# Kernel tuning notes

Measured on AMD Instinct MI355X. Metric: run time of the kernel, lower is better.

The kernel has to match this reference:

```python
import jax, jax.numpy as jnp
import numpy as np

NEG_INF = -1e9  # Keras uses a large negative for masked logits


def setup_inputs() -> dict:
    key = jax.random.key(0)
    k1, k2, k3, k4, k5 = jax.random.split(key, 5)
    B, Tq, Tv, D, U = 8, 128, 128, 512, 1024
    query = jax.random.normal(k1, (B, Tq, D), dtype=jnp.float32)
    value = jax.random.normal(k2, (B, Tv, D), dtype=jnp.float32)
    mask = jnp.ones((B, Tv), dtype=bool)
    # Dense(units, use_bias=False) kernels and AdditiveAttention scale vector
    W1 = jax.random.normal(k3, (D, U), dtype=jnp.float32) * (1.0 / np.sqrt(D))
    W2 = jax.random.normal(k4, (D, U), dtype=jnp.float32) * (1.0 / np.sqrt(D))
    scale = jax.random.normal(k5, (U,), dtype=jnp.float32) * (1.0 / np.sqrt(U))
    return {"query": query, "value": value, "mask": mask,
            "W1": W1, "W2": W2, "scale": scale}


def reference(query, value, mask, W1, W2, scale):
    # Projections (Dense, no bias)
    wq = jnp.einsum('btd,du->btu', query, W1)   # [B, Tq, U]
    wk = jnp.einsum('bsd,du->bsu', value, W2)   # [B, Tv, U]
    # Additive (Bahdanau) scores: sum_u scale_u * tanh(wq + wk)
    # Materializes [B, Tq, Tv, U] broadcast-add like Keras AdditiveAttention.
    scores = jnp.einsum('u,btsu->bts', scale,
                        jnp.tanh(wq[:, :, None, :] + wk[:, None, :, :]))
    # value mask over key axis (query_mask is all-ones in the source -> no-op)
    scores = jnp.where(mask[:, None, :], scores, NEG_INF)
    attn = jax.nn.softmax(scores, axis=-1)       # [B, Tq, Tv]
    context = jnp.einsum('bts,bsd->btd', attn, value)  # [B, Tq, D]
    return context, attn
```

## Files before the change

### kernel.cpp

```cpp
#include <hip/hip_runtime.h>

#define B_  8
#define TQ  128
#define TV  128
#define DIM 512
#define UU  1024
#define NSPLIT 16
#define NP  (B_ * TQ * TV)
#define C2  2.885390081777927f

typedef __attribute__((ext_vector_type(8))) short     short8;
typedef __attribute__((ext_vector_type(4))) float     f32x4;
typedef __attribute__((ext_vector_type(4))) unsigned short us4;

__device__ __forceinline__ unsigned short bf16_rtne(float x) {
    unsigned u = __float_as_uint(x);
    unsigned r = u + 0x7FFF + ((u >> 16) & 1);
    return (unsigned short)(r >> 16);
}

__global__ __launch_bounds__(256) void k_prep(
    const float* __restrict__ Q, const float* __restrict__ Vv,
    const float* __restrict__ W1, const float* __restrict__ W2,
    unsigned short* __restrict__ Ab, unsigned short* __restrict__ Wh)
{
    __shared__ float ts[32][36];
    const int bx = blockIdx.x;
    const int t  = threadIdx.x;

    if (bx < 1024) {
        int idx = bx * 256 + t;
        int mat = idx >> 17;
        const float* src = mat ? Vv : Q;
        int off = (idx & 131071) * 4;
        float4 v = *(const float4*)&src[off];
        us4 h;
        h.x = bf16_rtne(v.x);
        h.y = bf16_rtne(v.y);
        h.z = bf16_rtne(v.z);
        h.w = bf16_rtne(v.w);
        *(us4*)&Ab[mat * 524288 + off] = h;
    } else {
        int b2   = bx - 1024;
        int mat  = b2 >> 9;
        int tile = b2 & 511;
        int n0 = (tile & 31) * 32;
        int k0 = (tile >> 5) * 32;
        const float* W = mat ? W2 : W1;

        int kk = t >> 3, n4 = (t & 7) * 4;
        float4 w = *(const float4*)&W[(k0 + kk) * UU + n0 + n4];
        ts[n4 + 0][kk] = w.x; ts[n4 + 1][kk] = w.y;
        ts[n4 + 2][kk] = w.z; ts[n4 + 3][kk] = w.w;
        __syncthreads();

        int nn = t >> 3, k4 = (t & 7) * 4;
        float4 v = *(const float4*)&ts[nn][k4];
        us4 h;
        h.x = bf16_rtne(v.x);
        h.y = bf16_rtne(v.y);
        h.z = bf16_rtne(v.z);
        h.w = bf16_rtne(v.w);
        unsigned off = mat * 524288 + (n0 + nn) * 512 + k0 + k4;
        *(us4*)&Wh[off] = h;
    }
}

#define PKP 72
__global__ __launch_bounds__(256) void k_proj(
    const unsigned short* __restrict__ Ab, const unsigned short* __restrict__ Bh,
    float* __restrict__ Eq, float* __restrict__ Ek)
{
    __shared__ short sAb[64 * PKP], sBh[64 * PKP];

    const int tid  = threadIdx.x;
    const int wave = tid >> 6;
    const int lane = tid & 63;

    const int flat = blockIdx.x;
    const int x    = flat & 7;
    const int j    = flat >> 3;
    const int pair = x * 4 + (j >> 4);
    const int nt   = pair & 15;
    const int mat  = pair >> 4;
    const int mt   = j & 15;
    const int m0   = mt * 64;
    const int n0   = nt * 64;

    const unsigned mb = mat * 524288u;
    const int wm = (wave & 1) * 32;
    const int wn = (wave >> 1) * 32;

    const int sm = tid >> 2, sg = tid & 3;
    const unsigned short* gA = Ab + mb + (m0 + sm) * 512;
    const unsigned short* gB = Bh + mb + (n0 + sm) * 512;
    const int so0 = sm * PKP + sg * 8;
    const int so1 = sm * PKP + 32 + sg * 8;

    const int fr = lane & 15, fq = lane >> 4;
    const int aOff0 = (wm + fr) * PKP + fq * 8;
    const int aOff1 = (wm + 16 + fr) * PKP + fq * 8;
    const int bOff0 = (wn + fr) * PKP + fq * 8;
    const int bOff1 = (wn + 16 + fr) * PKP + fq * 8;

    f32x4 acc00 = {0.f, 0.f, 0.f, 0.f};
    f32x4 acc01 = {0.f, 0.f, 0.f, 0.f};
    f32x4 acc10 = {0.f, 0.f, 0.f, 0.f};
    f32x4 acc11 = {0.f, 0.f, 0.f, 0.f};

    int4 rA0, rA1, rB0, rB1;
    #define LOADALL(K)                                                       \
        rA0 = *(const int4*)(gA + (K) + sg * 8);                             \
        rA1 = *(const int4*)(gA + (K) + 32 + sg * 8);                        \
        rB0 = *(const int4*)(gB + (K) + sg * 8);                             \
        rB1 = *(const int4*)(gB + (K) + 32 + sg * 8);

    LOADALL(0)

    #pragma unroll 1
    for (int kc = 0; kc < 8; ++kc) {
        *(int4*)&sAb[so0] = rA0;  *(int4*)&sAb[so1] = rA1;
        *(int4*)&sBh[so0] = rB0;  *(int4*)&sBh[so1] = rB1;
        __syncthreads();

        if (kc < 7) { LOADALL((kc + 1) * 64) }

        #pragma unroll
        for (int ks = 0; ks < 2; ++ks) {
            const int o = ks * 32;
            short8 a0 = *(const short8*)&sAb[aOff0 + o];
            short8 a1 = *(const short8*)&sAb[aOff1 + o];
            short8 b0 = *(const short8*)&sBh[bOff0 + o];
            short8 b1 = *(const short8*)&sBh[bOff1 + o];

            acc00 = __builtin_amdgcn_mfma_f32_16x16x32_bf16(a0, b0, acc00, 0, 0, 0);
            acc01 = __builtin_amdgcn_mfma_f32_16x16x32_bf16(a0, b1, acc01, 0, 0, 0);
            acc10 = __builtin_amdgcn_mfma_f32_16x16x32_bf16(a1, b0, acc10, 0, 0, 0);
            acc11 = __builtin_amdgcn_mfma_f32_16x16x32_bf16(a1, b1, acc11, 0, 0, 0);
        }
        __syncthreads();
    }
    #undef LOADALL

    float* C = mat ? Ek : Eq;
    #pragma unroll
    for (int r = 0; r < 4; ++r) {
        int row0 = m0 + wm + fq * 4 + r;
        int row1 = row0 + 16;
        int col0 = n0 + wn + fr;
        C[row0 * UU + col0]      = __builtin_amdgcn_exp2f(C2 * acc00[r]);
        C[row0 * UU + col0 + 16] = __builtin_amdgcn_exp2f(C2 * acc01[r]);
        C[row1 * UU + col0]      = __builtin_amdgcn_exp2f(C2 * acc10[r]);
        C[row1 * UU + col0 + 16] = __builtin_amdgcn_exp2f(C2 * acc11[r]);
    }
}
#undef PKP

__global__ __launch_bounds__(256) void k_scores(
    const float* __restrict__ Eq, const float* __restrict__ Ek,
    const float* __restrict__ scale, float* __restrict__ part)
{
    __shared__ float qs[64][68];
    __shared__ float ks[64][68];
    __shared__ float ss[64];

    const int tid = threadIdx.x;
    const int tx  = tid & 15;
    const int ty  = tid >> 4;
    const int b   = blockIdx.z & 7;
    const int us  = blockIdx.z >> 3;
    const int t0  = blockIdx.y * 64;
    const int s0  = blockIdx.x * 64;
    const int u0  = us * (UU / NSPLIT);

    {
        const int r  = tid >> 2;
        const int c0 = (tid & 3) * 16;
        const float* srq = &Eq[(b * TQ + t0 + r) * UU + u0 + c0];
        const float* srk = &Ek[(b * TV + s0 + r) * UU + u0 + c0];
        const int rp = (r >> 2) | ((r & 3) << 4);
        #pragma unroll
        for (int i = 0; i < 4; ++i) {
            *(float4*)&qs[r][c0 + i * 4]  = *(const float4*)(srq + i * 4);
            *(float4*)&ks[rp][c0 + i * 4] = *(const float4*)(srk + i * 4);
        }
        if (tid < 16)
            *(float4*)&ss[tid * 4] = *(const float4*)&scale[u0 + tid * 4];
    }
    __syncthreads();

    float acc[4][4] = {};

    #pragma unroll 2
    for (int u4 = 0; u4 < 16; ++u4) {
        float4 q[4], k[4];
        #pragma unroll
        for (int i = 0; i < 4; ++i)
            q[i] = *(const float4*)&qs[ty * 4 + i][u4 * 4];
        #pragma unroll
        for (int jj = 0; jj < 4; ++jj)
            k[jj] = *(const float4*)&ks[tx + (jj << 4)][u4 * 4];
        float4 sv = *(const float4*)&ss[u4 * 4];

        #pragma unroll
        for (int i = 0; i < 4; ++i) {
            #pragma unroll
            for (int jj = 0; jj < 4; ++jj) {
                float p1 = q[i].x * k[jj].x, p2 = q[i].y * k[jj].y;
                float b1 = p1 + 1.f,        b2 = p2 + 1.f;
                float n1 = fmaf(sv.y, b1, sv.x * b2);
                acc[i][jj] = fmaf(n1, __builtin_amdgcn_rcpf(b1 * b2), acc[i][jj]);
                float p3 = q[i].z * k[jj].z, p4 = q[i].w * k[jj].w;
                float b3 = p3 + 1.f,        b4 = p4 + 1.f;
                float n2 = fmaf(sv.w, b3, sv.z * b4);
                acc[i][jj] = fmaf(n2, __builtin_amdgcn_rcpf(b3 * b4), acc[i][jj]);
            }
        }
    }

    #pragma unroll
    for (int i = 0; i < 4; ++i) {
        float4 o = {acc[i][0], acc[i][1], acc[i][2], acc[i][3]};
        *(float4*)&part[us * NP + (b * TQ + t0 + ty * 4 + i) * TV + s0 + tx * 4] = o;
    }
}

__global__ __launch_bounds__(256) void k_ctx(
    const float* __restrict__ part, const int* __restrict__ mask,
    const float* __restrict__ Vv,
    float* __restrict__ attn, float* __restrict__ ctx)
{
    __shared__ float at[128][12];

    const int tid = threadIdx.x;
    const int dc  = blockIdx.x;
    const int tt  = blockIdx.y;
    const int b   = blockIdx.z;
    const int t0  = tt * 8;
    const int rg  = tid >> 5;
    const int ln  = tid & 31;
    const int base = (b * TQ + t0 + rg) * TV;

    float x[4];
    #pragma unroll
    for (int j = 0; j < 4; ++j) {
        const int s = ln + 32 * j;
        float p = 0.f;
        #pragma unroll
        for (int i = 0; i < NSPLIT; ++i) p += part[i * NP + base + s];
        x[j] = mask[b * TV + s] ? -2.f * p : -1e9f;
    }
    float m = fmaxf(fmaxf(x[0], x[1]), fmaxf(x[2], x[3]));
    #pragma unroll
    for (int o = 16; o > 0; o >>= 1) m = fmaxf(m, __shfl_xor(m, o, 64));
    const float L2E = 1.4426950408889634f;
    float e[4], sum = 0.f;
    #pragma unroll
    for (int j = 0; j < 4; ++j) {
        e[j] = __builtin_amdgcn_exp2f((x[j] - m) * L2E);
        sum += e[j];
    }
    #pragma unroll
    for (int o = 16; o > 0; o >>= 1) sum += __shfl_xor(sum, o, 64);
    const float r = __builtin_amdgcn_rcpf(sum);
    #pragma unroll
    for (int j = 0; j < 4; ++j) {
        const float a = e[j] * r;
        at[ln + 32 * j][rg] = a;
        if (dc == 0) attn[base + ln + 32 * j] = a;
    }
    __syncthreads();

    const int d  = (tid & 127) + dc * 128;
    const int tg = tid >> 7;
    float acc[4] = {};
    const float* vp = &Vv[b * TV * DIM + d];
    #pragma unroll 4
    for (int s = 0; s < TV; ++s) {
        float v  = vp[s * DIM];
        float4 a = *(const float4*)&at[s][tg * 4];
        acc[0] = fmaf(a.x, v, acc[0]);
        acc[1] = fmaf(a.y, v, acc[1]);
        acc[2] = fmaf(a.z, v, acc[2]);
        acc[3] = fmaf(a.w, v, acc[3]);
    }
    #pragma unroll
    for (int j = 0; j < 4; ++j) {
        int t = t0 + tg * 4 + j;
        ctx[(b * TQ + t) * DIM + d] = acc[j];
    }
}

extern "C" void kernel_launch(void* const* d_in, const int* in_sizes, int n_in,
                              void* d_out, int out_size, void* d_ws, size_t ws_size,
                              hipStream_t stream)
{
    const float* query = (const float*)d_in[0];
    const float* value = (const float*)d_in[1];
    const int*   mask  = (const int*)d_in[2];
    const float* W1    = (const float*)d_in[3];
    const float* W2    = (const float*)d_in[4];
    const float* scale = (const float*)d_in[5];

    float* out  = (float*)d_out;
    float* ctx  = out;
    float* attn = out + B_ * TQ * DIM;

    float* Eq   = (float*)d_ws;
    float* Ek   = Eq + 1024 * 1024;
    float* part = Ek + 1024 * 1024;
    unsigned short* Ab = (unsigned short*)(part + NSPLIT * NP);
    unsigned short* Wh = Ab + 2 * 1024 * 512;

    hipLaunchKernelGGL(k_prep,   dim3(2048),             dim3(256), 0, stream,
                       query, value, W1, W2, Ab, Wh);
    hipLaunchKernelGGL(k_proj,   dim3(512),              dim3(256), 0, stream,
                       Ab, Wh, Eq, Ek);
    hipLaunchKernelGGL(k_scores, dim3(2, 2, 8 * NSPLIT), dim3(256), 0, stream,
                       Eq, Ek, scale, part);
    hipLaunchKernelGGL(k_ctx,    dim3(4, 16, 8),         dim3(256), 0, stream,
                       part, mask, value, attn, ctx);
}
```

Measured before the change: 109.9 us.

## Double threads per block in scores and context kernels, vectorize partial reduction

The scores kernel now runs 512 threads per block, each computing a 2x4 output tile instead of 4x4, with fused multiply-add for the tanh-rational terms. The context kernel handles 16 query rows per 512-thread block and reads partial sums and mask as float4/int4 vectors. The aim is more wavefronts to hide latency and fewer memory transactions, at the cost of less register-level reuse per thread in the scores kernel.

```diff
diff --git a/kernel.cpp b/kernel.cpp
--- a/kernel.cpp
+++ b/kernel.cpp
@@ -156,7 +156,7 @@
 }
 #undef PKP
 
-__global__ __launch_bounds__(256) void k_scores(
+__global__ __launch_bounds__(512, 4) void k_scores(
     const float* __restrict__ Eq, const float* __restrict__ Ek,
     const float* __restrict__ scale, float* __restrict__ part)
 {
@@ -174,44 +174,42 @@
     const int u0  = us * (UU / NSPLIT);
 
     {
-        const int r  = tid >> 2;
-        const int c0 = (tid & 3) * 16;
+        const int r  = tid >> 3;
+        const int c0 = (tid & 7) * 8;
         const float* srq = &Eq[(b * TQ + t0 + r) * UU + u0 + c0];
         const float* srk = &Ek[(b * TV + s0 + r) * UU + u0 + c0];
         const int rp = (r >> 2) | ((r & 3) << 4);
-        #pragma unroll
-        for (int i = 0; i < 4; ++i) {
-            *(float4*)&qs[r][c0 + i * 4]  = *(const float4*)(srq + i * 4);
-            *(float4*)&ks[rp][c0 + i * 4] = *(const float4*)(srk + i * 4);
-        }
+        *(float4*)&qs[r][c0]      = *(const float4*)(srq);
+        *(float4*)&qs[r][c0 + 4]  = *(const float4*)(srq + 4);
+        *(float4*)&ks[rp][c0]     = *(const float4*)(srk);
+        *(float4*)&ks[rp][c0 + 4] = *(const float4*)(srk + 4);
         if (tid < 16)
             *(float4*)&ss[tid * 4] = *(const float4*)&scale[u0 + tid * 4];
     }
     __syncthreads();
 
-    float acc[4][4] = {};
+    float acc[2][4] = {};
 
     #pragma unroll 2
     for (int u4 = 0; u4 < 16; ++u4) {
-        float4 q[4], k[4];
-        #pragma unroll
-        for (int i = 0; i < 4; ++i)
-            q[i] = *(const float4*)&qs[ty * 4 + i][u4 * 4];
+        float4 q[2], k[4];
+        q[0] = *(const float4*)&qs[ty * 2][u4 * 4];
+        q[1] = *(const float4*)&qs[ty * 2 + 1][u4 * 4];
         #pragma unroll
         for (int jj = 0; jj < 4; ++jj)
             k[jj] = *(const float4*)&ks[tx + (jj << 4)][u4 * 4];
         float4 sv = *(const float4*)&ss[u4 * 4];
 
         #pragma unroll
-        for (int i = 0; i < 4; ++i) {
+        for (int i = 0; i < 2; ++i) {
             #pragma unroll
             for (int jj = 0; jj < 4; ++jj) {
-                float p1 = q[i].x * k[jj].x, p2 = q[i].y * k[jj].y;
-                float b1 = p1 + 1.f,        b2 = p2 + 1.f;
+                float b1 = fmaf(q[i].x, k[jj].x, 1.f);
+                float b2 = fmaf(q[i].y, k[jj].y, 1.f);
                 float n1 = fmaf(sv.y, b1, sv.x * b2);
                 acc[i][jj] = fmaf(n1, __builtin_amdgcn_rcpf(b1 * b2), acc[i][jj]);
-                float p3 = q[i].z * k[jj].z, p4 = q[i].w * k[jj].w;
-                float b3 = p3 + 1.f,        b4 = p4 + 1.f;
+                float b3 = fmaf(q[i].z, k[jj].z, 1.f);
+                float b4 = fmaf(q[i].w, k[jj].w, 1.f);
                 float n2 = fmaf(sv.w, b3, sv.z * b4);
                 acc[i][jj] = fmaf(n2, __builtin_amdgcn_rcpf(b3 * b4), acc[i][jj]);
             }
@@ -219,40 +217,45 @@
     }
 
     #pragma unroll
-    for (int i = 0; i < 4; ++i) {
+    for (int i = 0; i < 2; ++i) {
         float4 o = {acc[i][0], acc[i][1], acc[i][2], acc[i][3]};
-        *(float4*)&part[us * NP + (b * TQ + t0 + ty * 4 + i) * TV + s0 + tx * 4] = o;
-    }
-}
-
-__global__ __launch_bounds__(256) void k_ctx(
+        *(float4*)&part[us * NP + (b * TQ + t0 + ty * 2 + i) * TV + s0 + tx * 4] = o;
+    }
+}
+
+__global__ __launch_bounds__(512) void k_ctx(
     const float* __restrict__ part, const int* __restrict__ mask,
     const float* __restrict__ Vv,
     float* __restrict__ attn, float* __restrict__ ctx)
 {
-    __shared__ float at[128][12];
+    __shared__ float at[128][20];
 
     const int tid = threadIdx.x;
     const int dc  = blockIdx.x;
     const int tt  = blockIdx.y;
     const int b   = blockIdx.z;
-    const int t0  = tt * 8;
-    const int rg  = tid >> 5;
-    const int ln  = tid & 31;
+    const int t0  = tt * 16;
+
+    const int rg = tid >> 5;
+    const int ln = tid & 31;
     const int base = (b * TQ + t0 + rg) * TV;
 
+    float4 p4 = {0.f, 0.f, 0.f, 0.f};
+    #pragma unroll
+    for (int i = 0; i < NSPLIT; ++i) {
+        float4 v = *(const float4*)&part[i * NP + base + ln * 4];
+        p4.x += v.x; p4.y += v.y; p4.z += v.z; p4.w += v.w;
+    }
+    const int4 mk = *(const int4*)&mask[b * TV + ln * 4];
     float x[4];
-    #pragma unroll
-    for (int j = 0; j < 4; ++j) {
-        const int s = ln + 32 * j;
-        float p = 0.f;
-        #pragma unroll
-        for (int i = 0; i < NSPLIT; ++i) p += part[i * NP + base + s];
-        x[j] = mask[b * TV + s] ? -2.f * p : -1e9f;
-    }
+    x[0] = mk.x ? -2.f * p4.x : -1e9f;
+    x[1] = mk.y ? -2.f * p4.y : -1e9f;
+    x[2] = mk.z ? -2.f * p4.z : -1e9f;
+    x[3] = mk.w ? -2.f * p4.w : -1e9f;
+
     float m = fmaxf(fmaxf(x[0], x[1]), fmaxf(x[2], x[3]));
     #pragma unroll
-    for (int o = 16; o > 0; o >>= 1) m = fmaxf(m, __shfl_xor(m, o, 64));
+    for (int o = 16; o > 0; o >>= 1) m = fmaxf(m, __shfl_xor(m, o, 32));
     const float L2E = 1.4426950408889634f;
     float e[4], sum = 0.f;
     #pragma unroll
@@ -261,14 +264,15 @@
         sum += e[j];
     }
     #pragma unroll
-    for (int o = 16; o > 0; o >>= 1) sum += __shfl_xor(sum, o, 64);
+    for (int o = 16; o > 0; o >>= 1) sum += __shfl_xor(sum, o, 32);
     const float r = __builtin_amdgcn_rcpf(sum);
-    #pragma unroll
-    for (int j = 0; j < 4; ++j) {
-        const float a = e[j] * r;
-        at[ln + 32 * j][rg] = a;
-        if (dc == 0) attn[base + ln + 32 * j] = a;
-    }
+
+    float4 av = {e[0] * r, e[1] * r, e[2] * r, e[3] * r};
+    at[ln * 4 + 0][rg] = av.x;
+    at[ln * 4 + 1][rg] = av.y;
+    at[ln * 4 + 2][rg] = av.z;
+    at[ln * 4 + 3][rg] = av.w;
+    if (dc == 0) *(float4*)&attn[base + ln * 4] = av;
     __syncthreads();
 
     const int d  = (tid & 127) + dc * 128;
@@ -316,8 +320,8 @@
                        query, value, W1, W2, Ab, Wh);
     hipLaunchKernelGGL(k_proj,   dim3(512),              dim3(256), 0, stream,
                        Ab, Wh, Eq, Ek);
-    hipLaunchKernelGGL(k_scores, dim3(2, 2, 8 * NSPLIT), dim3(256), 0, stream,
+    hipLaunchKernelGGL(k_scores, dim3(2, 2, 8 * NSPLIT), dim3(512), 0, stream,
                        Eq, Ek, scale, part);
-    hipLaunchKernelGGL(k_ctx,    dim3(4, 16, 8),         dim3(256), 0, stream,
+    hipLaunchKernelGGL(k_ctx,    dim3(4, 8, 8),          dim3(512), 0, stream,
                        part, mask, value, attn, ctx);
 }
```

Measured after the change: 110.3 us. Within noise of the previous version (+0.3%).

## Fuse bf16 conversion into projection and merge scores, softmax, context kernels

Applied to the files above, without the earlier changes.

Removes the separate prep kernel by converting fp32 inputs and weights to bf16 inside the projection GEMM's shared-memory staging, with the weight transpose done through scalar LDS stores. Also fuses the score, softmax and context stages into one kernel per (batch, 4-query block), using packed f32x2 FMA for the score math. This drops the split-U partial buffer and two launches. The trade-off is fewer blocks (256) and each block redoing the full U=1024 reduction serially, with every block reloading Ek for its batch.

```diff
diff --git a/kernel.cpp b/kernel.cpp
--- a/kernel.cpp
+++ b/kernel.cpp
@@ -5,12 +5,11 @@
 #define TV  128
 #define DIM 512
 #define UU  1024
-#define NSPLIT 16
-#define NP  (B_ * TQ * TV)
 #define C2  2.885390081777927f
 
 typedef __attribute__((ext_vector_type(8))) short     short8;
 typedef __attribute__((ext_vector_type(4))) float     f32x4;
+typedef __attribute__((ext_vector_type(2))) float     f32x2;
 typedef __attribute__((ext_vector_type(4))) unsigned short us4;
 
 __device__ __forceinline__ unsigned short bf16_rtne(float x) {
@@ -19,56 +18,23 @@
     return (unsigned short)(r >> 16);
 }
 
-__global__ __launch_bounds__(256) void k_prep(
+__device__ __forceinline__ us4 cvt4(float4 v) {
+    us4 h;
+    h.x = bf16_rtne(v.x);
+    h.y = bf16_rtne(v.y);
+    h.z = bf16_rtne(v.z);
+    h.w = bf16_rtne(v.w);
+    return h;
+}
+
+__device__ __forceinline__ f32x2 pkfma(f32x2 a, f32x2 b, f32x2 c) {
+    return __builtin_elementwise_fma(a, b, c);
+}
+
+#define PKP 72
+__global__ __launch_bounds__(256, 2) void k_proj(
     const float* __restrict__ Q, const float* __restrict__ Vv,
     const float* __restrict__ W1, const float* __restrict__ W2,
-    unsigned short* __restrict__ Ab, unsigned short* __restrict__ Wh)
-{
-    __shared__ float ts[32][36];
-    const int bx = blockIdx.x;
-    const int t  = threadIdx.x;
-
-    if (bx < 1024) {
-        int idx = bx * 256 + t;
-        int mat = idx >> 17;
-        const float* src = mat ? Vv : Q;
-        int off = (idx & 131071) * 4;
-        float4 v = *(const float4*)&src[off];
-        us4 h;
-        h.x = bf16_rtne(v.x);
-        h.y = bf16_rtne(v.y);
-        h.z = bf16_rtne(v.z);
-        h.w = bf16_rtne(v.w);
-        *(us4*)&Ab[mat * 524288 + off] = h;
-    } else {
-        int b2   = bx - 1024;
-        int mat  = b2 >> 9;
-        int tile = b2 & 511;
-        int n0 = (tile & 31) * 32;
-        int k0 = (tile >> 5) * 32;
-        const float* W = mat ? W2 : W1;
-
-        int kk = t >> 3, n4 = (t & 7) * 4;
-        float4 w = *(const float4*)&W[(k0 + kk) * UU + n0 + n4];
-        ts[n4 + 0][kk] = w.x; ts[n4 + 1][kk] = w.y;
-        ts[n4 + 2][kk] = w.z; ts[n4 + 3][kk] = w.w;
-        __syncthreads();
-
-        int nn = t >> 3, k4 = (t & 7) * 4;
-        float4 v = *(const float4*)&ts[nn][k4];
-        us4 h;
-        h.x = bf16_rtne(v.x);
-        h.y = bf16_rtne(v.y);
-        h.z = bf16_rtne(v.z);
-        h.w = bf16_rtne(v.w);
-        unsigned off = mat * 524288 + (n0 + nn) * 512 + k0 + k4;
-        *(us4*)&Wh[off] = h;
-    }
-}
-
-#define PKP 72
-__global__ __launch_bounds__(256) void k_proj(
-    const unsigned short* __restrict__ Ab, const unsigned short* __restrict__ Bh,
     float* __restrict__ Eq, float* __restrict__ Ek)
 {
     __shared__ short sAb[64 * PKP], sBh[64 * PKP];
@@ -87,15 +53,19 @@
     const int m0   = mt * 64;
     const int n0   = nt * 64;
 
-    const unsigned mb = mat * 524288u;
+    const float* Asrc = mat ? Vv : Q;
+    const float* Wsrc = mat ? W2 : W1;
+
     const int wm = (wave & 1) * 32;
     const int wn = (wave >> 1) * 32;
 
     const int sm = tid >> 2, sg = tid & 3;
-    const unsigned short* gA = Ab + mb + (m0 + sm) * 512;
-    const unsigned short* gB = Bh + mb + (n0 + sm) * 512;
+    const float* gA = Asrc + (m0 + sm) * 512;
     const int so0 = sm * PKP + sg * 8;
     const int so1 = sm * PKP + 32 + sg * 8;
+
+    const int kk = tid & 63, ng = tid >> 6;
+    const float* gW = Wsrc + n0 + ng * 16;
 
     const int fr = lane & 15, fq = lane >> 4;
     const int aOff0 = (wm + fr) * PKP + fq * 8;
@@ -108,19 +78,38 @@
     f32x4 acc10 = {0.f, 0.f, 0.f, 0.f};
     f32x4 acc11 = {0.f, 0.f, 0.f, 0.f};
 
-    int4 rA0, rA1, rB0, rB1;
+    float4 a0, a1, a2, a3, w0, w1, w2, w3;
     #define LOADALL(K)                                                       \
-        rA0 = *(const int4*)(gA + (K) + sg * 8);                             \
-        rA1 = *(const int4*)(gA + (K) + 32 + sg * 8);                        \
-        rB0 = *(const int4*)(gB + (K) + sg * 8);                             \
-        rB1 = *(const int4*)(gB + (K) + 32 + sg * 8);
+        a0 = *(const float4*)(gA + (K) + sg * 8);                            \
+        a1 = *(const float4*)(gA + (K) + sg * 8 + 4);                        \
+        a2 = *(const float4*)(gA + (K) + 32 + sg * 8);                       \
+        a3 = *(const float4*)(gA + (K) + 32 + sg * 8 + 4);                   \
+        {                                                                    \
+            const float* wr = gW + ((K) + kk) * UU;                          \
+            w0 = *(const float4*)(wr);                                       \
+            w1 = *(const float4*)(wr + 4);                                   \
+            w2 = *(const float4*)(wr + 8);                                   \
+            w3 = *(const float4*)(wr + 12);                                  \
+        }
 
     LOADALL(0)
 
     #pragma unroll 1
     for (int kc = 0; kc < 8; ++kc) {
-        *(int4*)&sAb[so0] = rA0;  *(int4*)&sAb[so1] = rA1;
-        *(int4*)&sBh[so0] = rB0;  *(int4*)&sBh[so1] = rB1;
+        *(us4*)&sAb[so0]     = cvt4(a0);
+        *(us4*)&sAb[so0 + 4] = cvt4(a1);
+        *(us4*)&sAb[so1]     = cvt4(a2);
+        *(us4*)&sAb[so1 + 4] = cvt4(a3);
+        {
+            us4 h[4] = {cvt4(w0), cvt4(w1), cvt4(w2), cvt4(w3)};
+            #pragma unroll
+            for (int g = 0; g < 4; ++g) {
+                sBh[(ng * 16 + g * 4 + 0) * PKP + kk] = (short)h[g].x;
+                sBh[(ng * 16 + g * 4 + 1) * PKP + kk] = (short)h[g].y;
+                sBh[(ng * 16 + g * 4 + 2) * PKP + kk] = (short)h[g].z;
+                sBh[(ng * 16 + g * 4 + 3) * PKP + kk] = (short)h[g].w;
+            }
+        }
         __syncthreads();
 
         if (kc < 7) { LOADALL((kc + 1) * 64) }
@@ -128,15 +117,15 @@
         #pragma unroll
         for (int ks = 0; ks < 2; ++ks) {
             const int o = ks * 32;
-            short8 a0 = *(const short8*)&sAb[aOff0 + o];
-            short8 a1 = *(const short8*)&sAb[aOff1 + o];
-            short8 b0 = *(const short8*)&sBh[bOff0 + o];
-            short8 b1 = *(const short8*)&sBh[bOff1 + o];
-
-            acc00 = __builtin_amdgcn_mfma_f32_16x16x32_bf16(a0, b0, acc00, 0, 0, 0);
-            acc01 = __builtin_amdgcn_mfma_f32_16x16x32_bf16(a0, b1, acc01, 0, 0, 0);
-            acc10 = __builtin_amdgcn_mfma_f32_16x16x32_bf16(a1, b0, acc10, 0, 0, 0);
-            acc11 = __builtin_amdgcn_mfma_f32_16x16x32_bf16(a1, b1, acc11, 0, 0, 0);
+            short8 fa0 = *(const short8*)&sAb[aOff0 + o];
+            short8 fa1 = *(const short8*)&sAb[aOff1 + o];
+            short8 fb0 = *(const short8*)&sBh[bOff0 + o];
+            short8 fb1 = *(const short8*)&sBh[bOff1 + o];
+
+            acc00 = __builtin_amdgcn_mfma_f32_16x16x32_bf16(fa0, fb0, acc00, 0, 0, 0);
+            acc01 = __builtin_amdgcn_mfma_f32_16x16x32_bf16(fa0, fb1, acc01, 0, 0, 0);
+            acc10 = __builtin_amdgcn_mfma_f32_16x16x32_bf16(fa1, fb0, acc10, 0, 0, 0);
+            acc11 = __builtin_amdgcn_mfma_f32_16x16x32_bf16(fa1, fb1, acc11, 0, 0, 0);
         }
         __syncthreads();
     }
@@ -156,140 +145,124 @@
 }
 #undef PKP
 
-__global__ __launch_bounds__(256) void k_scores(
+#define EKP 132
+__global__ __launch_bounds__(256, 2) void k_sac(
     const float* __restrict__ Eq, const float* __restrict__ Ek,
-    const float* __restrict__ scale, float* __restrict__ part)
-{
-    __shared__ float qs[64][68];
-    __shared__ float ks[64][68];
-    __shared__ float ss[64];
-
-    const int tid = threadIdx.x;
-    const int tx  = tid & 15;
-    const int ty  = tid >> 4;
-    const int b   = blockIdx.z & 7;
-    const int us  = blockIdx.z >> 3;
-    const int t0  = blockIdx.y * 64;
-    const int s0  = blockIdx.x * 64;
-    const int u0  = us * (UU / NSPLIT);
-
-    {
-        const int r  = tid >> 2;
-        const int c0 = (tid & 3) * 16;
-        const float* srq = &Eq[(b * TQ + t0 + r) * UU + u0 + c0];
-        const float* srk = &Ek[(b * TV + s0 + r) * UU + u0 + c0];
-        const int rp = (r >> 2) | ((r & 3) << 4);
-        #pragma unroll
-        for (int i = 0; i < 4; ++i) {
-            *(float4*)&qs[r][c0 + i * 4]  = *(const float4*)(srq + i * 4);
-            *(float4*)&ks[rp][c0 + i * 4] = *(const float4*)(srk + i * 4);
-        }
-        if (tid < 16)
-            *(float4*)&ss[tid * 4] = *(const float4*)&scale[u0 + tid * 4];
-    }
-    __syncthreads();
-
-    float acc[4][4] = {};
-
-    #pragma unroll 2
-    for (int u4 = 0; u4 < 16; ++u4) {
-        float4 q[4], k[4];
-        #pragma unroll
-        for (int i = 0; i < 4; ++i)
-            q[i] = *(const float4*)&qs[ty * 4 + i][u4 * 4];
-        #pragma unroll
-        for (int jj = 0; jj < 4; ++jj)
-            k[jj] = *(const float4*)&ks[tx + (jj << 4)][u4 * 4];
-        float4 sv = *(const float4*)&ss[u4 * 4];
-
-        #pragma unroll
-        for (int i = 0; i < 4; ++i) {
-            #pragma unroll
-            for (int jj = 0; jj < 4; ++jj) {
-                float p1 = q[i].x * k[jj].x, p2 = q[i].y * k[jj].y;
-                float b1 = p1 + 1.f,        b2 = p2 + 1.f;
-                float n1 = fmaf(sv.y, b1, sv.x * b2);
-                acc[i][jj] = fmaf(n1, __builtin_amdgcn_rcpf(b1 * b2), acc[i][jj]);
-                float p3 = q[i].z * k[jj].z, p4 = q[i].w * k[jj].w;
-                float b3 = p3 + 1.f,        b4 = p4 + 1.f;
-                float n2 = fmaf(sv.w, b3, sv.z * b4);
-                acc[i][jj] = fmaf(n2, __builtin_amdgcn_rcpf(b3 * b4), acc[i][jj]);
-            }
-        }
-    }
-
-    #pragma unroll
-    for (int i = 0; i < 4; ++i) {
-        float4 o = {acc[i][0], acc[i][1], acc[i][2], acc[i][3]};
-        *(float4*)&part[us * NP + (b * TQ + t0 + ty * 4 + i) * TV + s0 + tx * 4] = o;
-    }
-}
-
-__global__ __launch_bounds__(256) void k_ctx(
-    const float* __restrict__ part, const int* __restrict__ mask,
+    const float* __restrict__ scale, const int* __restrict__ mask,
     const float* __restrict__ Vv,
     float* __restrict__ attn, float* __restrict__ ctx)
 {
-    __shared__ float at[128][12];
+    __shared__ float ek2[64][EKP];
+    __shared__ float qs[4][68];
+    __shared__ float ss[64];
+    __shared__ float at[4][132];
 
     const int tid = threadIdx.x;
-    const int dc  = blockIdx.x;
-    const int tt  = blockIdx.y;
-    const int b   = blockIdx.z;
-    const int t0  = tt * 8;
-    const int rg  = tid >> 5;
-    const int ln  = tid & 31;
-    const int base = (b * TQ + t0 + rg) * TV;
-
-    float x[4];
+    const int bid = blockIdx.x;
+    const int b   = bid & 7;
+    const int t0  = (bid >> 3) * 4;
+    const int sp  = tid & 63;
+    const int tq  = tid >> 6;
+
+    const int uu = tid >> 6;
+    const float* ekrow0 = &Ek[(b * TV + 2 * sp) * UU + uu * 16];
+    const float* ekrow1 = ekrow0 + UU;
+
+    f32x2 acc = {0.f, 0.f};
+    const f32x2 one2 = {1.f, 1.f};
+
+    #pragma unroll 1
+    for (int uc = 0; uc < 16; ++uc) {
+        const int u0 = uc * 64;
+        if (uc) __syncthreads();
+        #pragma unroll
+        for (int c = 0; c < 4; ++c) {
+            float4 ra = *(const float4*)(ekrow0 + u0 + c * 4);
+            float4 rb = *(const float4*)(ekrow1 + u0 + c * 4);
+            float4 lo = {ra.x, rb.x, ra.y, rb.y};
+            float4 hi = {ra.z, rb.z, ra.w, rb.w};
+            *(float4*)&ek2[sp][(uu * 16 + c * 4) * 2]     = lo;
+            *(float4*)&ek2[sp][(uu * 16 + c * 4) * 2 + 4] = hi;
+        }
+        if (tid < 64) {
+            const int r = tid >> 4, cs = (tid & 15) * 4;
+            *(float4*)&qs[r][cs] =
+                *(const float4*)&Eq[(b * TQ + t0 + r) * UU + u0 + cs];
+        }
+        if (tid < 16)
+            *(float4*)&ss[tid * 4] = *(const float4*)&scale[u0 + tid * 4];
+        __syncthreads();
+
+        #pragma unroll 4
+        for (int u4 = 0; u4 < 16; ++u4) {
+            float4 ka = *(const float4*)&ek2[sp][u4 * 8];
+            float4 kb = *(const float4*)&ek2[sp][u4 * 8 + 4];
+            f32x2 kA0 = {ka.x, ka.y}, kA1 = {ka.z, ka.w};
+            f32x2 kA2 = {kb.x, kb.y}, kA3 = {kb.z, kb.w};
+            float4 qv = *(const float4*)&qs[tq][u4 * 4];
+            float4 sv = *(const float4*)&ss[u4 * 4];
+
+            f32x2 b1 = pkfma((f32x2){qv.x, qv.x}, kA0, one2);
+            f32x2 b2 = pkfma((f32x2){qv.y, qv.y}, kA1, one2);
+            f32x2 p  = b1 * b2;
+            f32x2 n  = pkfma((f32x2){sv.y, sv.y}, b1,
+                             (f32x2){sv.x, sv.x} * b2);
+            f32x2 r  = {__builtin_amdgcn_rcpf(p.x),
+                        __builtin_amdgcn_rcpf(p.y)};
+            acc = pkfma(n, r, acc);
+
+            f32x2 b3 = pkfma((f32x2){qv.z, qv.z}, kA2, one2);
+            f32x2 b4 = pkfma((f32x2){qv.w, qv.w}, kA3, one2);
+            f32x2 p2 = b3 * b4;
+            f32x2 n2 = pkfma((f32x2){sv.w, sv.w}, b3,
+                             (f32x2){sv.z, sv.z} * b4);
+            f32x2 r2 = {__builtin_amdgcn_rcpf(p2.x),
+                        __builtin_amdgcn_rcpf(p2.y)};
+            acc = pkfma(n2, r2, acc);
+        }
+    }
+
+    const int2 mk = *(const int2*)&mask[b * TV + 2 * sp];
+    float x0 = mk.x ? -2.f * acc.x : -1e9f;
+    float x1 = mk.y ? -2.f * acc.y : -1e9f;
+    float m = fmaxf(x0, x1);
     #pragma unroll
-    for (int j = 0; j < 4; ++j) {
-        const int s = ln + 32 * j;
-        float p = 0.f;
-        #pragma unroll
-        for (int i = 0; i < NSPLIT; ++i) p += part[i * NP + base + s];
-        x[j] = mask[b * TV + s] ? -2.f * p : -1e9f;
-    }
-    float m = fmaxf(fmaxf(x[0], x[1]), fmaxf(x[2], x[3]));
+    for (int o = 32; o > 0; o >>= 1) m = fmaxf(m, __shfl_xor(m, o, 64));
+    const float L2E = 1.4426950408889634f;
+    float e0 = __builtin_amdgcn_exp2f((x0 - m) * L2E);
+    float e1 = __builtin_amdgcn_exp2f((x1 - m) * L2E);
+    float sum = e0 + e1;
     #pragma unroll
-    for (int o = 16; o > 0; o >>= 1) m = fmaxf(m, __shfl_xor(m, o, 64));
-    const float L2E = 1.4426950408889634f;
-    float e[4], sum = 0.f;
-    #pragma unroll
-    for (int j = 0; j < 4; ++j) {
-        e[j] = __builtin_amdgcn_exp2f((x[j] - m) * L2E);
-        sum += e[j];
-    }
-    #pragma unroll
-    for (int o = 16; o > 0; o >>= 1) sum += __shfl_xor(sum, o, 64);
-    const float r = __builtin_amdgcn_rcpf(sum);
-    #pragma unroll
-    for (int j = 0; j < 4; ++j) {
-        const float a = e[j] * r;
-        at[ln + 32 * j][rg] = a;
-        if (dc == 0) attn[base + ln + 32 * j] = a;
-    }
+    for (int o = 32; o > 0; o >>= 1) sum += __shfl_xor(sum, o, 64);
+    const float rs = __builtin_amdgcn_rcpf(sum);
+    const float av0 = e0 * rs, av1 = e1 * rs;
+
+    const int trow = t0 + tq;
+    *(float2*)&attn[(b * TQ + trow) * TV + 2 * sp] = (float2){av0, av1};
+    at[tq][2 * sp]     = av0;
+    at[tq][2 * sp + 1] = av1;
     __syncthreads();
 
-    const int d  = (tid & 127) + dc * 128;
-    const int tg = tid >> 7;
-    float acc[4] = {};
-    const float* vp = &Vv[b * TV * DIM + d];
+    const int tr = tid >> 6;
+    const int dl = (tid & 63) * 8;
+    float c0 = 0.f, c1 = 0.f, c2 = 0.f, c3 = 0.f;
+    float c4 = 0.f, c5 = 0.f, c6 = 0.f, c7 = 0.f;
+    const float* vp = &Vv[b * TV * DIM + dl];
     #pragma unroll 4
     for (int s = 0; s < TV; ++s) {
-        float v  = vp[s * DIM];
-        float4 a = *(const float4*)&at[s][tg * 4];
-        acc[0] = fmaf(a.x, v, acc[0]);
-        acc[1] = fmaf(a.y, v, acc[1]);
-        acc[2] = fmaf(a.z, v, acc[2]);
-        acc[3] = fmaf(a.w, v, acc[3]);
-    }
-    #pragma unroll
-    for (int j = 0; j < 4; ++j) {
-        int t = t0 + tg * 4 + j;
-        ctx[(b * TQ + t) * DIM + d] = acc[j];
-    }
-}
+        float a  = at[tr][s];
+        float4 v0 = *(const float4*)(vp + s * DIM);
+        float4 v1 = *(const float4*)(vp + s * DIM + 4);
+        c0 = fmaf(a, v0.x, c0); c1 = fmaf(a, v0.y, c1);
+        c2 = fmaf(a, v0.z, c2); c3 = fmaf(a, v0.w, c3);
+        c4 = fmaf(a, v1.x, c4); c5 = fmaf(a, v1.y, c5);
+        c6 = fmaf(a, v1.z, c6); c7 = fmaf(a, v1.w, c7);
+    }
+    float* cp = &ctx[(b * TQ + t0 + tr) * DIM + dl];
+    *(float4*)(cp)     = (float4){c0, c1, c2, c3};
+    *(float4*)(cp + 4) = (float4){c4, c5, c6, c7};
+}
+#undef EKP
 
 extern "C" void kernel_launch(void* const* d_in, const int* in_sizes, int n_in,
                               void* d_out, int out_size, void* d_ws, size_t ws_size,
@@ -306,18 +279,11 @@
     float* ctx  = out;
     float* attn = out + B_ * TQ * DIM;
 
-    float* Eq   = (float*)d_ws;
-    float* Ek   = Eq + 1024 * 1024;
-    float* part = Ek + 1024 * 1024;
-    unsigned short* Ab = (unsigned short*)(part + NSPLIT * NP);
-    unsigned short* Wh = Ab + 2 * 1024 * 512;
-
-    hipLaunchKernelGGL(k_prep,   dim3(2048),             dim3(256), 0, stream,
-                       query, value, W1, W2, Ab, Wh);
-    hipLaunchKernelGGL(k_proj,   dim3(512),              dim3(256), 0, stream,
-                       Ab, Wh, Eq, Ek);
-    hipLaunchKernelGGL(k_scores, dim3(2, 2, 8 * NSPLIT), dim3(256), 0, stream,
-                       Eq, Ek, scale, part);
-    hipLaunchKernelGGL(k_ctx,    dim3(4, 16, 8),         dim3(256), 0, stream,
-                       part, mask, value, attn, ctx);
-}
+    float* Eq = (float*)d_ws;
+    float* Ek = Eq + 1024 * 1024;
+
+    hipLaunchKernelGGL(k_proj, dim3(512), dim3(256), 0, stream,
+                       query, value, W1, W2, Eq, Ek);
+    hipLaunchKernelGGL(k_sac,  dim3(256), dim3(256), 0, stream,
+                       Eq, Ek, scale, mask, value, attn, ctx);
+}
```

Measured after the change: 140.6 us. 1.28x slower.
